# Optimization experiments

Hardware: AMD Instinct MI355X
Metric: run time of the kernel (lower is better)

Reference implementation:

```python
import jax, jax.numpy as jnp
import numpy as np

B, F, T = 16, 257, 4000
FRAME_LEN = 512
HOP = 256
NFFT = 512  # 2**ceil(log2(frame_len))
EPS = float(np.finfo(np.float32).eps)


def _sqrthann(n):
    i = jnp.arange(n, dtype=jnp.float32)
    hann = 0.5 * (1.0 - jnp.cos(2.0 * jnp.pi * i / n))  # periodic hann
    return jnp.sqrt(hann)


def setup_inputs() -> dict:
    key = jax.random.key(0)
    transform = jax.random.normal(key, (B, F, T, 2), dtype=jnp.float32)
    window = _sqrthann(FRAME_LEN)
    return {"transform": transform, "window": window}


def reference(transform, window):
    # transform: [B, F=257, T, 2] (real/imag), window: [512]
    real = transform[..., 0]  # [B,257,T]
    imag = transform[..., 1]
    # onesided -> mirror to full 512 bins (Hermitian symmetry)
    nb = NFFT // 2  # 256
    real_full = jnp.concatenate([real, real[:, nb - 1:0:-1, :]], axis=1)   # [B,512,T]
    imag_full = jnp.concatenate([imag, -imag[:, nb - 1:0:-1, :]], axis=1)  # [B,512,T]
    # inverse DFT kernel (matches init_kernel with inverse=True, not normalized):
    # kernel[k, n] = cos(2*pi*k*n/N)/N (real part), -sin(...)/N (imag part)
    k = jnp.arange(NFFT, dtype=jnp.float32)
    ang = (2.0 * np.pi / NFFT) * (k[:, None] * k[None, :])  # [512,512]
    C = jnp.cos(ang) / NFFT
    S = -jnp.sin(ang) / NFFT
    # per-frame time signal: real iDFT, then apply synthesis window
    frames = jnp.einsum('bkt,kn->btn', real_full, C) + jnp.einsum('bkt,kn->btn', imag_full, S)  # [B,T,512]
    frames = frames * window  # broadcast over last dim
    # overlap-add
    out_len = (T - 1) * HOP + FRAME_LEN
    idx = jnp.arange(T)[:, None] * HOP + jnp.arange(FRAME_LEN)[None, :]  # [T,512]
    wav = jnp.zeros((frames.shape[0], out_len), dtype=frames.dtype).at[:, idx].add(frames)  # [B,S]
    # window-power normalization (overlap-added window^2)
    w2 = jnp.broadcast_to(window ** 2, (T, FRAME_LEN))
    denorm = jnp.zeros((out_len,), dtype=frames.dtype).at[idx.reshape(-1)].add(w2.reshape(-1))
    return wav / (denorm + EPS)
```

## Files before the change

### kernel.cpp

```cpp
#include <hip/hip_runtime.h>
#include <stdint.h>


#define EPS_F 1.1920928955078125e-07f
#define TWO_PI_OVER_512 1.2271846303085130e-02f

typedef __bf16 bf16x8 __attribute__((ext_vector_type(8)));
typedef float f32x4 __attribute__((ext_vector_type(4)));

__device__ __forceinline__ uint16_t f2bf_bits(float x) {
  return __builtin_bit_cast(uint16_t, (__bf16)x);
}
__device__ __forceinline__ float bf2f_bits(uint16_t u) {
  return (float)__builtin_bit_cast(__bf16, u);
}

#define GLOAD16(srcp, dstp)                                                   \
  __builtin_amdgcn_global_load_lds(                                          \
      (const __attribute__((address_space(1))) uint32_t*)(srcp),             \
      (__attribute__((address_space(3))) uint32_t*)(dstp), 16, 0, 0)

__global__ void build_table_kernel(uint8_t* __restrict__ tb) {
  const int k = blockIdx.x;
  const int g = k >> 3;
  const int n = threadIdx.x;
  float v = 0.0f;
  int f, c, valid;
  if (k < 288) {
    const int fe = k >> 1;
    c = k & 1; f = 2 * fe; valid = (fe <= 128);
  } else {
    const int ko = k - 288;
    c = ko & 1; f = 2 * (ko >> 1) + 1; valid = 1;
  }
  if (valid) {
    const float s = (f == 0 || f == 256) ? 1.0f : 2.0f;
    const int a = (f * n) & 511;
    const float th = (float)a * TWO_PI_OVER_512;
    const float tr = c ? -sinf(th) : cosf(th);
    v = s * tr * (1.0f / 512.0f);
  }
  const int off = (((g * 256 + n) << 4) ^ ((g & 3) << 5)) + ((k & 7) << 1);
  *(uint16_t*)(tb + off) = f2bf_bits(v);
}

__device__ __forceinline__ float rd_sf(const uint8_t* sF, int col, int row2) {
  return bf2f_bits(*(const uint16_t*)(
      sF + col * 72 + ((row2 * 2) ^ (((col >> 4) & 3) << 2))));
}

__global__ __launch_bounds__(512, 4)
void istft_fused_kernel(const float2* __restrict__ in,
                        const float* __restrict__ win,
                        const uint8_t* __restrict__ tb,
                        float* __restrict__ out) {
  __shared__ __align__(1024) uint8_t smem[36864];
  uint8_t* sB = smem;
  uint8_t* sF = smem;

  const int tid  = threadIdx.x;
  const int lane = tid & 63;
  const int wave = tid >> 6;
  const int wn   = wave & 3;
  const int wm   = wave >> 2;
  const int l15  = lane & 15;
  const int g    = lane >> 4;
  const int b  = blockIdx.y;
  const int ib = blockIdx.x;
  const int t0 = (ib == 63) ? 3936 : ib * 63;

  f32x4 accE[2][4], accO[2][4];
#pragma unroll
  for (int mi = 0; mi < 2; ++mi)
#pragma unroll
    for (int nj = 0; nj < 4; ++nj) {
      accE[mi][nj] = (f32x4){0.f, 0.f, 0.f, 0.f};
      accO[mi][nj] = (f32x4){0.f, 0.f, 0.f, 0.f};
    }

  const long inBase = (long)b * (257L * 4000);
  const long tARow  = inBase + (t0 + wm * 32 + l15);

  float2 q[2][8];

#define ISSUE_A(KS)                                                           \
  {                                                                           \
    float2* qd = q[(KS) & 1];                                                 \
    _Pragma("unroll") for (int mi = 0; mi < 2; ++mi)                          \
    _Pragma("unroll") for (int p = 0; p < 4; ++p) {                           \
      int f;                                                                  \
      if ((KS) < 9) {                                                         \
        int fe = (KS) * 16 + g * 4 + p;                                       \
        if (fe > 128) fe = 128;                                               \
        f = 2 * fe;                                                           \
      } else {                                                                \
        f = 2 * (((KS) - 9) * 16 + g * 4 + p) + 1;                            \
      }                                                                       \
      qd[mi * 4 + p] = in[tARow + mi * 16 + (long)f * 4000];                  \
    }                                                                         \
  }
#define ISSUE_B(T)                                                            \
  {                                                                           \
    const uint8_t* src = tb + (T) * 16384 + wave * 2048 + lane * 16;          \
    uint8_t* dst = sB + ((T) & 1) * 16384 + wave * 2048 + lane * 16;          \
    GLOAD16(src, dst);                                                        \
    GLOAD16(src + 1024, dst + 1024);                                          \
  }
#define MFMA_STEP(ACC)                                                        \
  _Pragma("unroll") for (int nj = 0; nj < 4; ++nj) {                          \
    const bf16x8 bfr = *(const bf16x8*)(sBc + nbase + (nj << 8));             \
    ACC[0][nj] = __builtin_amdgcn_mfma_f32_16x16x32_bf16(af[0], bfr,          \
                                                         ACC[0][nj], 0, 0, 0);\
    ACC[1][nj] = __builtin_amdgcn_mfma_f32_16x16x32_bf16(af[1], bfr,          \
                                                         ACC[1][nj], 0, 0, 0);\
  }

  ISSUE_B(0);
  __builtin_amdgcn_sched_barrier(0);
  ISSUE_A(0);
  __builtin_amdgcn_sched_barrier(0);
  ISSUE_A(1);
  __builtin_amdgcn_sched_barrier(0);

  const int nbase = ((g * 256 + wn * 64 + l15) << 4) ^ (g << 5);

#pragma unroll
  for (int ks = 0; ks < 17; ++ks) {
    if (ks < 16)
      asm volatile("s_waitcnt vmcnt(8)" ::: "memory");
    else
      asm volatile("s_waitcnt vmcnt(0)" ::: "memory");
    __builtin_amdgcn_s_barrier();
    __builtin_amdgcn_sched_barrier(0);

    if (ks < 16) {
      ISSUE_B(ks + 1);
    }
    __builtin_amdgcn_sched_barrier(0);

    bf16x8 af[2];
#pragma unroll
    for (int mi = 0; mi < 2; ++mi) {
      bf16x8 a;
#pragma unroll
      for (int p = 0; p < 4; ++p) {
        const float2 v = q[ks & 1][mi * 4 + p];
        a[2 * p]     = (__bf16)v.x;
        a[2 * p + 1] = (__bf16)v.y;
      }
      af[mi] = a;
    }
    __builtin_amdgcn_sched_barrier(0);
    if (ks < 15) {
      ISSUE_A(ks + 2);
    }
    __builtin_amdgcn_sched_barrier(0);

    const uint8_t* sBc = sB + (ks & 1) * 16384;
    if (ks < 9) {
      MFMA_STEP(accE);
    } else {
      MFMA_STEP(accO);
    }
  }

  __syncthreads();
  float* outb = out + (long)b * 1024256;
  const float invd = 1.0f / (1.0f + EPS_F);

  float wL[4], wR[4];
#pragma unroll
  for (int nj = 0; nj < 4; ++nj) {
    wL[nj] = win[wn * 64 + nj * 16 + l15];
    wR[nj] = win[wn * 64 + nj * 16 + l15 + 256];
  }

#define STAGE_PASS()                                                          \
  {                                                                           \
    _Pragma("unroll")                                                         \
    for (int mi = 0; mi < 2; ++mi) {                                          \
      const int q4 = mi * 16 + (g << 2);             \
      _Pragma("unroll")                                                       \
      for (int nj = 0; nj < 4; ++nj) {                                        \
        const int colL = wn * 64 + nj * 16 + l15;                             \
        const int colR = colL + 256;                                          \
        const int swzL = ((colL >> 4) & 3) << 2;                              \
        const int swzR = ((colR >> 4) & 3) << 2;                              \
        const f32x4 e = accE[mi][nj];                                         \
        const f32x4 o = accO[mi][nj];                                         \
        const float wl = wL[nj], wr = wR[nj];                                 \
        uint32_t lo = (uint32_t)f2bf_bits((e[0] + o[0]) * wl) |               \
                      ((uint32_t)f2bf_bits((e[1] + o[1]) * wl) << 16);        \
        uint32_t hi = (uint32_t)f2bf_bits((e[2] + o[2]) * wl) |               \
                      ((uint32_t)f2bf_bits((e[3] + o[3]) * wl) << 16);        \
        *(uint32_t*)(sF + colL * 72 + ((q4 * 2) ^ swzL))       = lo;          \
        *(uint32_t*)(sF + colL * 72 + (((q4 + 2) * 2) ^ swzL)) = hi;          \
        lo = (uint32_t)f2bf_bits((e[0] - o[0]) * wr) |                        \
             ((uint32_t)f2bf_bits((e[1] - o[1]) * wr) << 16);                 \
        hi = (uint32_t)f2bf_bits((e[2] - o[2]) * wr) |                        \
             ((uint32_t)f2bf_bits((e[3] - o[3]) * wr) << 16);                 \
        *(uint32_t*)(sF + colR * 72 + ((q4 * 2) ^ swzR))       = lo;          \
        *(uint32_t*)(sF + colR * 72 + (((q4 + 2) * 2) ^ swzR)) = hi;          \
      }                                                                       \
    }                                                                         \
  }

  if (wm == 0) STAGE_PASS();
  __syncthreads();
#pragma unroll 1
  for (int i = tid; i < 31 * 256; i += 512) {
    const int cl = 1 + (i >> 8);
    const int r  = i & 255;
    const float v0 = rd_sf(sF, 256 + r, cl - 1);
    const float v1 = rd_sf(sF, r, cl);
    outb[(t0 + cl) * 256 + r] = (v0 + v1) * invd;
  }
  if (ib == 0 && tid < 256) {
    const float w = win[tid];
    outb[tid] = rd_sf(sF, tid, 0) / (w * w + EPS_F);
  }
  const float vsave = (tid < 256) ? rd_sf(sF, 256 + tid, 31) : 0.0f;
  __syncthreads();
  if (wm == 1) STAGE_PASS();
  __syncthreads();
  if (tid < 256)
    outb[(t0 + 32) * 256 + tid] = (vsave + rd_sf(sF, tid, 0)) * invd;
#pragma unroll 1
  for (int i = tid; i < 31 * 256; i += 512) {
    const int cl = 33 + (i >> 8);
    const int r  = i & 255;
    const float v0 = rd_sf(sF, 256 + r, cl - 33);
    const float v1 = rd_sf(sF, r, cl - 32);
    outb[(t0 + cl) * 256 + r] = (v0 + v1) * invd;
  }
  if (ib == 63 && tid < 256) {
    const float w = win[256 + tid];
    outb[1024000 + tid] = rd_sf(sF, 256 + tid, 31) / (w * w + EPS_F);
  }
}

extern "C" void kernel_launch(void* const* d_in, const int* in_sizes, int n_in,
                              void* d_out, int out_size, void* d_ws, size_t ws_size,
                              hipStream_t stream) {
  (void)in_sizes; (void)n_in; (void)out_size; (void)ws_size;
  const float2* tr = (const float2*)d_in[0];
  const float* win = (const float*)d_in[1];
  uint8_t* tb = (uint8_t*)d_ws;
  build_table_kernel<<<dim3(544), dim3(256), 0, stream>>>(tb);
  istft_fused_kernel<<<dim3(64, 16), dim3(512), 0, stream>>>(tr, win, tb,
                                                             (float*)d_out);
}
```

Measured before the change: 70.34 us.

## Shrink ISTFT blocks to 16 frames with 256 threads for more parallelism

Reduces each block's frame tile from 64 to 16 frames (stride 15) and the block from 512 to 256 threads, launching about four times as many blocks. Each wave now computes one 16-row M tile, and the overlap-add epilogue becomes a single unswizzled LDS staging pass. The aim is better occupancy and load balance and less epilogue serialization. The cost is that the DFT table is reloaded into LDS for every 16 frames and more boundary frames are recomputed.

```diff
diff --git a/kernel.cpp b/kernel.cpp
--- a/kernel.cpp
+++ b/kernel.cpp
@@ -44,49 +44,43 @@
   *(uint16_t*)(tb + off) = f2bf_bits(v);
 }
 
-__device__ __forceinline__ float rd_sf(const uint8_t* sF, int col, int row2) {
-  return bf2f_bits(*(const uint16_t*)(
-      sF + col * 72 + ((row2 * 2) ^ (((col >> 4) & 3) << 2))));
-}
-
-__global__ __launch_bounds__(512, 4)
+__device__ __forceinline__ float rd_sf(const uint8_t* sF, int col, int row) {
+  return bf2f_bits(*(const uint16_t*)(sF + col * 36 + row * 2));
+}
+
+__global__ __launch_bounds__(256, 5)
 void istft_fused_kernel(const float2* __restrict__ in,
                         const float* __restrict__ win,
                         const uint8_t* __restrict__ tb,
                         float* __restrict__ out) {
-  __shared__ __align__(1024) uint8_t smem[36864];
+  __shared__ __align__(1024) uint8_t smem[32768];
   uint8_t* sB = smem;
   uint8_t* sF = smem;
 
   const int tid  = threadIdx.x;
   const int lane = tid & 63;
   const int wave = tid >> 6;
-  const int wn   = wave & 3;
-  const int wm   = wave >> 2;
   const int l15  = lane & 15;
   const int g    = lane >> 4;
   const int b  = blockIdx.y;
   const int ib = blockIdx.x;
-  const int t0 = (ib == 63) ? 3936 : ib * 63;
-
-  f32x4 accE[2][4], accO[2][4];
-#pragma unroll
-  for (int mi = 0; mi < 2; ++mi)
-#pragma unroll
-    for (int nj = 0; nj < 4; ++nj) {
-      accE[mi][nj] = (f32x4){0.f, 0.f, 0.f, 0.f};
-      accO[mi][nj] = (f32x4){0.f, 0.f, 0.f, 0.f};
-    }
+  const int t0 = (ib == 266) ? 3984 : ib * 15;
+
+  f32x4 accE[4], accO[4];
+#pragma unroll
+  for (int nj = 0; nj < 4; ++nj) {
+    accE[nj] = (f32x4){0.f, 0.f, 0.f, 0.f};
+    accO[nj] = (f32x4){0.f, 0.f, 0.f, 0.f};
+  }
 
   const long inBase = (long)b * (257L * 4000);
-  const long tARow  = inBase + (t0 + wm * 32 + l15);
-
-  float2 q[2][8];
+  const long tcol   = inBase + (t0 + l15);
+
+  float2 q[2][4];
 
 #define ISSUE_A(KS)                                                           \
   {                                                                           \
     float2* qd = q[(KS) & 1];                                                 \
-    _Pragma("unroll") for (int mi = 0; mi < 2; ++mi)                          \
     _Pragma("unroll") for (int p = 0; p < 4; ++p) {                           \
       int f;                                                                  \
       if ((KS) < 9) {                                                         \
@@ -96,23 +90,15 @@
       } else {                                                                \
         f = 2 * (((KS) - 9) * 16 + g * 4 + p) + 1;                            \
       }                                                                       \
-      qd[mi * 4 + p] = in[tARow + mi * 16 + (long)f * 4000];                  \
+      qd[p] = in[tcol + (long)f * 4000];                                      \
     }                                                                         \
   }
 #define ISSUE_B(T)                                                            \
   {                                                                           \
-    const uint8_t* src = tb + (T) * 16384 + wave * 2048 + lane * 16;          \
-    uint8_t* dst = sB + ((T) & 1) * 16384 + wave * 2048 + lane * 16;          \
-    GLOAD16(src, dst);                                                        \
-    GLOAD16(src + 1024, dst + 1024);                                          \
-  }
-#define MFMA_STEP(ACC)                                                        \
-  _Pragma("unroll") for (int nj = 0; nj < 4; ++nj) {                          \
-    const bf16x8 bfr = *(const bf16x8*)(sBc + nbase + (nj << 8));             \
-    ACC[0][nj] = __builtin_amdgcn_mfma_f32_16x16x32_bf16(af[0], bfr,          \
-                                                         ACC[0][nj], 0, 0, 0);\
-    ACC[1][nj] = __builtin_amdgcn_mfma_f32_16x16x32_bf16(af[1], bfr,          \
-                                                         ACC[1][nj], 0, 0, 0);\
+    const uint8_t* src = tb + (T) * 16384 + wave * 4096 + lane * 16;          \
+    uint8_t* dst = sB + ((T) & 1) * 16384 + wave * 4096 + lane * 16;          \
+    _Pragma("unroll") for (int c = 0; c < 4; ++c)                             \
+      GLOAD16(src + c * 1024, dst + c * 1024);                                \
   }
 
   ISSUE_B(0);
@@ -122,12 +108,12 @@
   ISSUE_A(1);
   __builtin_amdgcn_sched_barrier(0);
 
-  const int nbase = ((g * 256 + wn * 64 + l15) << 4) ^ (g << 5);
+  const int nbase = ((g * 256 + wave * 64 + l15) << 4) ^ (g << 5);
 
 #pragma unroll
   for (int ks = 0; ks < 17; ++ks) {
     if (ks < 16)
-      asm volatile("s_waitcnt vmcnt(8)" ::: "memory");
+      asm volatile("s_waitcnt vmcnt(4)" ::: "memory");
     else
       asm volatile("s_waitcnt vmcnt(0)" ::: "memory");
     __builtin_amdgcn_s_barrier();
@@ -138,17 +124,12 @@
     }
     __builtin_amdgcn_sched_barrier(0);
 
-    bf16x8 af[2];
-#pragma unroll
-    for (int mi = 0; mi < 2; ++mi) {
-      bf16x8 a;
-#pragma unroll
-      for (int p = 0; p < 4; ++p) {
-        const float2 v = q[ks & 1][mi * 4 + p];
-        a[2 * p]     = (__bf16)v.x;
-        a[2 * p + 1] = (__bf16)v.y;
-      }
-      af[mi] = a;
+    bf16x8 af;
+#pragma unroll
+    for (int p = 0; p < 4; ++p) {
+      const float2 v = q[ks & 1][p];
+      af[2 * p]     = (__bf16)v.x;
+      af[2 * p + 1] = (__bf16)v.y;
     }
     __builtin_amdgcn_sched_barrier(0);
     if (ks < 15) {
@@ -158,9 +139,19 @@
 
     const uint8_t* sBc = sB + (ks & 1) * 16384;
     if (ks < 9) {
-      MFMA_STEP(accE);
+#pragma unroll
+      for (int nj = 0; nj < 4; ++nj) {
+        const bf16x8 bfr = *(const bf16x8*)(sBc + nbase + (nj << 8));
+        accE[nj] = __builtin_amdgcn_mfma_f32_16x16x32_bf16(af, bfr,
+                                                           accE[nj], 0, 0, 0);
+      }
     } else {
-      MFMA_STEP(accO);
+#pragma unroll
+      for (int nj = 0; nj < 4; ++nj) {
+        const bf16x8 bfr = *(const bf16x8*)(sBc + nbase + (nj << 8));
+        accO[nj] = __builtin_amdgcn_mfma_f32_16x16x32_bf16(af, bfr,
+                                                           accO[nj], 0, 0, 0);
+      }
     }
   }
 
@@ -168,74 +159,44 @@
   float* outb = out + (long)b * 1024256;
   const float invd = 1.0f / (1.0f + EPS_F);
 
-  float wL[4], wR[4];
 #pragma unroll
   for (int nj = 0; nj < 4; ++nj) {
-    wL[nj] = win[wn * 64 + nj * 16 + l15];
-    wR[nj] = win[wn * 64 + nj * 16 + l15 + 256];
-  }
-
-#define STAGE_PASS()                                                          \
-  {                                                                           \
-    _Pragma("unroll")                                                         \
-    for (int mi = 0; mi < 2; ++mi) {                                          \
-      const int q4 = mi * 16 + (g << 2);             \
-      _Pragma("unroll")                                                       \
-      for (int nj = 0; nj < 4; ++nj) {                                        \
-        const int colL = wn * 64 + nj * 16 + l15;                             \
-        const int colR = colL + 256;                                          \
-        const int swzL = ((colL >> 4) & 3) << 2;                              \
-        const int swzR = ((colR >> 4) & 3) << 2;                              \
-        const f32x4 e = accE[mi][nj];                                         \
-        const f32x4 o = accO[mi][nj];                                         \
-        const float wl = wL[nj], wr = wR[nj];                                 \
-        uint32_t lo = (uint32_t)f2bf_bits((e[0] + o[0]) * wl) |               \
-                      ((uint32_t)f2bf_bits((e[1] + o[1]) * wl) << 16);        \
-        uint32_t hi = (uint32_t)f2bf_bits((e[2] + o[2]) * wl) |               \
-                      ((uint32_t)f2bf_bits((e[3] + o[3]) * wl) << 16);        \
-        *(uint32_t*)(sF + colL * 72 + ((q4 * 2) ^ swzL))       = lo;          \
-        *(uint32_t*)(sF + colL * 72 + (((q4 + 2) * 2) ^ swzL)) = hi;          \
-        lo = (uint32_t)f2bf_bits((e[0] - o[0]) * wr) |                        \
-             ((uint32_t)f2bf_bits((e[1] - o[1]) * wr) << 16);                 \
-        hi = (uint32_t)f2bf_bits((e[2] - o[2]) * wr) |                        \
-             ((uint32_t)f2bf_bits((e[3] - o[3]) * wr) << 16);                 \
-        *(uint32_t*)(sF + colR * 72 + ((q4 * 2) ^ swzR))       = lo;          \
-        *(uint32_t*)(sF + colR * 72 + (((q4 + 2) * 2) ^ swzR)) = hi;          \
-      }                                                                       \
-    }                                                                         \
-  }
-
-  if (wm == 0) STAGE_PASS();
+    const int colL = wave * 64 + nj * 16 + l15;
+    const int colR = colL + 256;
+    const float wl = win[colL];
+    const float wr = win[colR];
+    const f32x4 e = accE[nj];
+    const f32x4 o = accO[nj];
+    uint32_t lo = (uint32_t)f2bf_bits((e[0] + o[0]) * wl) |
+                  ((uint32_t)f2bf_bits((e[1] + o[1]) * wl) << 16);
+    uint32_t hi = (uint32_t)f2bf_bits((e[2] + o[2]) * wl) |
+                  ((uint32_t)f2bf_bits((e[3] + o[3]) * wl) << 16);
+    *(uint32_t*)(sF + colL * 36 + g * 8)     = lo;
+    *(uint32_t*)(sF + colL * 36 + g * 8 + 4) = hi;
+    lo = (uint32_t)f2bf_bits((e[0] - o[0]) * wr) |
+         ((uint32_t)f2bf_bits((e[1] - o[1]) * wr) << 16);
+    hi = (uint32_t)f2bf_bits((e[2] - o[2]) * wr) |
+         ((uint32_t)f2bf_bits((e[3] - o[3]) * wr) << 16);
+    *(uint32_t*)(sF + colR * 36 + g * 8)     = lo;
+    *(uint32_t*)(sF + colR * 36 + g * 8 + 4) = hi;
+  }
   __syncthreads();
+
+  const int r = tid;
+  const int clmin = (ib == 266) ? 7 : 1;
 #pragma unroll 1
-  for (int i = tid; i < 31 * 256; i += 512) {
-    const int cl = 1 + (i >> 8);
-    const int r  = i & 255;
+  for (int cl = clmin; cl <= 15; ++cl) {
     const float v0 = rd_sf(sF, 256 + r, cl - 1);
     const float v1 = rd_sf(sF, r, cl);
     outb[(t0 + cl) * 256 + r] = (v0 + v1) * invd;
   }
-  if (ib == 0 && tid < 256) {
-    const float w = win[tid];
-    outb[tid] = rd_sf(sF, tid, 0) / (w * w + EPS_F);
-  }
-  const float vsave = (tid < 256) ? rd_sf(sF, 256 + tid, 31) : 0.0f;
-  __syncthreads();
-  if (wm == 1) STAGE_PASS();
-  __syncthreads();
-  if (tid < 256)
-    outb[(t0 + 32) * 256 + tid] = (vsave + rd_sf(sF, tid, 0)) * invd;
-#pragma unroll 1
-  for (int i = tid; i < 31 * 256; i += 512) {
-    const int cl = 33 + (i >> 8);
-    const int r  = i & 255;
-    const float v0 = rd_sf(sF, 256 + r, cl - 33);
-    const float v1 = rd_sf(sF, r, cl - 32);
-    outb[(t0 + cl) * 256 + r] = (v0 + v1) * invd;
-  }
-  if (ib == 63 && tid < 256) {
-    const float w = win[256 + tid];
-    outb[1024000 + tid] = rd_sf(sF, 256 + tid, 31) / (w * w + EPS_F);
+  if (ib == 0) {
+    const float w = win[r];
+    outb[r] = rd_sf(sF, r, 0) / (w * w + EPS_F);
+  }
+  if (ib == 266) {
+    const float w = win[256 + r];
+    outb[1024000 + r] = rd_sf(sF, 256 + r, 15) / (w * w + EPS_F);
   }
 }
 
@@ -247,6 +208,6 @@
   const float* win = (const float*)d_in[1];
   uint8_t* tb = (uint8_t*)d_ws;
   build_table_kernel<<<dim3(544), dim3(256), 0, stream>>>(tb);
-  istft_fused_kernel<<<dim3(64, 16), dim3(512), 0, stream>>>(tr, win, tb,
-                                                             (float*)d_out);
-}
+  istft_fused_kernel<<<dim3(267, 16), dim3(256), 0, stream>>>(tr, win, tb,
+                                                              (float*)d_out);
+}
```

Result: slower. 95.06 us (+35.1%).

## Stage A operand through LDS with coalesced time-contiguous loads and bf16 packing

Applied to the files above, without the earlier changes.

Each lane used to load its own float2 spectrum values, strided by frequency rows, straight into registers for the MFMA A fragments. Now each wave loads two frequency rows across 64 consecutive time columns, which is a coalesced pattern. It converts them to bf16 once and writes them to a double-buffered LDS tile, and the MFMA fragments are read back from LDS as 16-byte vectors. This cuts the number of scattered global loads and the per-lane register buffering, at the cost of more LDS space, extra LDS traffic, and more waitcnt/barrier coupling in the pipeline.

```diff
diff --git a/kernel.cpp b/kernel.cpp
--- a/kernel.cpp
+++ b/kernel.cpp
@@ -7,6 +7,7 @@
 
 typedef __bf16 bf16x8 __attribute__((ext_vector_type(8)));
 typedef float f32x4 __attribute__((ext_vector_type(4)));
+typedef uint32_t u32x2 __attribute__((ext_vector_type(2)));
 
 __device__ __forceinline__ uint16_t f2bf_bits(float x) {
   return __builtin_bit_cast(uint16_t, (__bf16)x);
@@ -54,8 +55,9 @@
                         const float* __restrict__ win,
                         const uint8_t* __restrict__ tb,
                         float* __restrict__ out) {
-  __shared__ __align__(1024) uint8_t smem[36864];
-  uint8_t* sB = smem;
+  __shared__ __align__(1024) uint8_t smem[43008];
+  uint8_t* sA = smem;
+  uint8_t* sB = smem + 10240;
   uint8_t* sF = smem;
 
   const int tid  = threadIdx.x;
@@ -79,25 +81,28 @@
     }
 
   const long inBase = (long)b * (257L * 4000);
-  const long tARow  = inBase + (t0 + wm * 32 + l15);
-
-  float2 q[2][8];
-
-#define ISSUE_A(KS)                                                           \
-  {                                                                           \
-    float2* qd = q[(KS) & 1];                                                 \
-    _Pragma("unroll") for (int mi = 0; mi < 2; ++mi)                          \
-    _Pragma("unroll") for (int p = 0; p < 4; ++p) {                           \
-      int f;                                                                  \
-      if ((KS) < 9) {                                                         \
-        int fe = (KS) * 16 + g * 4 + p;                                       \
-        if (fe > 128) fe = 128;                                               \
-        f = 2 * fe;                                                           \
-      } else {                                                                \
-        f = 2 * (((KS) - 9) * 16 + g * 4 + p) + 1;                            \
-      }                                                                       \
-      qd[mi * 4 + p] = in[tARow + mi * 16 + (long)f * 4000];                  \
-    }                                                                         \
+  const long tcol   = inBase + (t0 + lane);
+
+  float2 alq[2][2];
+
+#define A_GLOBAL_F(KS, FH)                                                    \
+  ((KS) < 9 ? 2 * ((((KS) * 16 + (FH)) > 128) ? 128 : ((KS) * 16 + (FH)))    \
+            : 2 * (((KS) - 9) * 16 + (FH)) + 1)
+#define ISSUE_AL(KS)                                                          \
+  {                                                                           \
+    const int fg0 = A_GLOBAL_F(KS, 2 * wave);                                 \
+    const int fg1 = A_GLOBAL_F(KS, 2 * wave + 1);                             \
+    alq[(KS) & 1][0] = in[tcol + (long)fg0 * 4000];                           \
+    alq[(KS) & 1][1] = in[tcol + (long)fg1 * 4000];                           \
+  }
+#define WRITE_A(KS)                                                           \
+  {                                                                           \
+    const float2 x = alq[(KS) & 1][0];                                        \
+    const float2 y = alq[(KS) & 1][1];                                        \
+    u32x2 wv;                                                                 \
+    wv[0] = (uint32_t)f2bf_bits(x.x) | ((uint32_t)f2bf_bits(x.y) << 16);      \
+    wv[1] = (uint32_t)f2bf_bits(y.x) | ((uint32_t)f2bf_bits(y.y) << 16);      \
+    *(u32x2*)(sA + ((KS) & 1) * 5120 + lane * 80 + wave * 8) = wv;            \
   }
 #define ISSUE_B(T)                                                            \
   {                                                                           \
@@ -115,11 +120,14 @@
                                                          ACC[1][nj], 0, 0, 0);\
   }
 
+  ISSUE_AL(0);
+  __builtin_amdgcn_sched_barrier(0);
   ISSUE_B(0);
   __builtin_amdgcn_sched_barrier(0);
-  ISSUE_A(0);
-  __builtin_amdgcn_sched_barrier(0);
-  ISSUE_A(1);
+  ISSUE_AL(1);
+  __builtin_amdgcn_sched_barrier(0);
+  asm volatile("s_waitcnt vmcnt(4)" ::: "memory");
+  WRITE_A(0);
   __builtin_amdgcn_sched_barrier(0);
 
   const int nbase = ((g * 256 + wn * 64 + l15) << 4) ^ (g << 5);
@@ -127,9 +135,9 @@
 #pragma unroll
   for (int ks = 0; ks < 17; ++ks) {
     if (ks < 16)
-      asm volatile("s_waitcnt vmcnt(8)" ::: "memory");
+      asm volatile("s_waitcnt vmcnt(2) lgkmcnt(0)" ::: "memory");
     else
-      asm volatile("s_waitcnt vmcnt(0)" ::: "memory");
+      asm volatile("s_waitcnt vmcnt(0) lgkmcnt(0)" ::: "memory");
     __builtin_amdgcn_s_barrier();
     __builtin_amdgcn_sched_barrier(0);
 
@@ -137,31 +145,34 @@
       ISSUE_B(ks + 1);
     }
     __builtin_amdgcn_sched_barrier(0);
-
+    if (ks < 15) {
+      ISSUE_AL(ks + 2);
+    }
+    __builtin_amdgcn_sched_barrier(0);
+
+    const uint8_t* sAc = sA + (ks & 1) * 5120;
     bf16x8 af[2];
 #pragma unroll
     for (int mi = 0; mi < 2; ++mi) {
-      bf16x8 a;
-#pragma unroll
-      for (int p = 0; p < 4; ++p) {
-        const float2 v = q[ks & 1][mi * 4 + p];
-        a[2 * p]     = (__bf16)v.x;
-        a[2 * p + 1] = (__bf16)v.y;
-      }
-      af[mi] = a;
-    }
-    __builtin_amdgcn_sched_barrier(0);
-    if (ks < 15) {
-      ISSUE_A(ks + 2);
-    }
-    __builtin_amdgcn_sched_barrier(0);
-
+      const int t = wm * 32 + mi * 16 + l15;
+      af[mi] = *(const bf16x8*)(sAc + t * 80 + g * 16);
+    }
     const uint8_t* sBc = sB + (ks & 1) * 16384;
     if (ks < 9) {
       MFMA_STEP(accE);
     } else {
       MFMA_STEP(accO);
     }
+    __builtin_amdgcn_sched_barrier(0);
+
+    if (ks < 15) {
+      asm volatile("s_waitcnt vmcnt(4)" ::: "memory");
+      WRITE_A(ks + 1);
+    } else if (ks == 15) {
+      asm volatile("s_waitcnt vmcnt(2)" ::: "memory");
+      WRITE_A(16);
+    }
+    __builtin_amdgcn_sched_barrier(0);
   }
 
   __syncthreads();
```

New measurement: 57.96 us (median of 3 runs). 1.21x faster.
